# Performance work log

Hardware: AMD Instinct MI355X
Metric: run time of the kernel (lower is better)

The kernel has to match this reference:

```python
import jax, jax.numpy as jnp
import numpy as np

N_USERS = 100000
N_ITEMS = 20000
N_GENRES = 20
N_TAGS = 1128
EMB_ID = 64
EMB_FEAT = 64
HEADS = 8
HIDDEN = 256
D_MOVIE = EMB_ID + 2 * EMB_FEAT  # 192
E_HALF = 200000
N_NODES = N_USERS + N_ITEMS
NEG_SLOPE = 0.2


def setup_inputs() -> dict:
    key = jax.random.key(0)
    ks = jax.random.split(key, 24)
    p = lambda k, shape: (jax.random.normal(k, shape, jnp.float32) * 0.05)
    user_ids = jnp.arange(N_USERS)
    movie_ids = jnp.arange(N_ITEMS)
    mov_x = jax.random.normal(ks[0], (N_ITEMS, N_GENRES + N_TAGS), jnp.float32)
    # bipartite user<->movie edges, both directions (no self loops, matches add_self_loops=False)
    u = jax.random.randint(ks[1], (E_HALF,), 0, N_USERS)
    m = jax.random.randint(ks[2], (E_HALF,), 0, N_ITEMS) + N_USERS
    edge_index = jnp.stack([jnp.concatenate([u, m]), jnp.concatenate([m, u])])  # [2, 2*E_HALF]
    C1 = HIDDEN // HEADS
    return dict(
        user_ids=user_ids, movie_ids=movie_ids, mov_x=mov_x, edge_index=edge_index,
        user_emb=p(ks[3], (N_USERS, EMB_ID)), item_emb=p(ks[4], (N_ITEMS, EMB_ID)),
        gW1=p(ks[5], (N_GENRES, EMB_FEAT)), gb1=jnp.zeros((EMB_FEAT,), jnp.float32),
        gW2=p(ks[6], (EMB_FEAT, EMB_FEAT)), gb2=jnp.zeros((EMB_FEAT,), jnp.float32),
        tW1=p(ks[7], (N_TAGS, EMB_FEAT)), tb1=jnp.zeros((EMB_FEAT,), jnp.float32),
        tW2=p(ks[8], (EMB_FEAT, EMB_FEAT)), tb2=jnp.zeros((EMB_FEAT,), jnp.float32),
        Ws1=p(ks[9], (D_MOVIE, HIDDEN)), Wd1=p(ks[10], (D_MOVIE, HIDDEN)),
        as1=p(ks[11], (HEADS, C1)), ad1=p(ks[12], (HEADS, C1)),
        b1=jnp.zeros((HIDDEN,), jnp.float32),
        Ws2=p(ks[13], (HIDDEN, HIDDEN)), Wd2=p(ks[14], (HIDDEN, HIDDEN)),
        as2=p(ks[15], (1, HIDDEN)), ad2=p(ks[16], (1, HIDDEN)),
        b2=jnp.zeros((HIDDEN,), jnp.float32),
    )


def _gat(x, edge_index, Ws, Wd, a_s, a_d, bias, concat):
    # PyG GATConv (eval mode: dropout off, add_self_loops=False)
    N = x.shape[0]
    H, C = a_s.shape
    hs = (x @ Ws).reshape(N, H, C)  # source-side projection
    hd = (x @ Wd).reshape(N, H, C)  # dest-side projection
    al_s = (hs * a_s).sum(-1)  # [N, H]
    al_d = (hd * a_d).sum(-1)  # [N, H]
    src, dst = edge_index[0], edge_index[1]
    e = al_s[src] + al_d[dst]                      # [E, H]
    e = jnp.where(e > 0, e, NEG_SLOPE * e)         # leaky_relu(0.2)
    mmax = jax.ops.segment_max(e, dst, num_segments=N)
    w = jnp.exp(e - mmax[dst])
    ssum = jax.ops.segment_sum(w, dst, num_segments=N)
    alpha = w / (ssum[dst] + 1e-16)                # segment softmax over incoming edges
    out = jax.ops.segment_sum(hs[src] * alpha[:, :, None], dst, num_segments=N)  # [N, H, C]
    out = out.reshape(N, H * C) if concat else out.mean(axis=1)
    return out + bias


def reference(user_ids, movie_ids, mov_x, edge_index,
              user_emb, item_emb,
              gW1, gb1, gW2, gb2, tW1, tb1, tW2, tb2,
              Ws1, Wd1, as1, ad1, b1,
              Ws2, Wd2, as2, ad2, b2):
    g_feat = mov_x[:, :N_GENRES]
    t_feat = mov_x[:, N_GENRES:]
    g = jax.nn.relu(g_feat @ gW1 + gb1) @ gW2 + gb2
    t = jax.nn.relu(t_feat @ tW1 + tb1) @ tW2 + tb2
    x_mov = jnp.concatenate([item_emb[movie_ids], g, t], axis=1)  # [n_m, D_MOVIE]
    # homogeneous graph: user nodes first (zero-pad user emb to D_MOVIE), then movies
    x_usr = jnp.pad(user_emb[user_ids], ((0, 0), (0, D_MOVIE - EMB_ID)))
    x = jnp.concatenate([x_usr, x_mov], axis=0)  # [N_NODES, D_MOVIE]
    out = jax.nn.elu(_gat(x, edge_index, Ws1, Wd1, as1, ad1, b1, concat=True))
    out = _gat(out, edge_index, Ws2, Wd2, as2, ad2, b2, concat=False)
    ptr = jnp.array([0, N_USERS, N_USERS + N_ITEMS])
    return out, ptr
```

## Files before the change

kernel.cpp:

```cpp
#include <hip/hip_runtime.h>
#include <hip/hip_bf16.h>

#define N_USERS_C 100000
#define N_ITEMS_C 20000
#define N_NODES_C 120000
#define E_TOT_C   400000
#define D_IN_C    192
#define HID_C     256
#define NEG_C     0.2f
#define CLAMP_C   1000.0f
#define KPAD_C    1152
#define NB_SCAN   ((N_NODES_C + 255) / 256)
#define ROWE      40

typedef __attribute__((ext_vector_type(8))) short bfrag;
typedef __attribute__((ext_vector_type(4))) float ffrag;

__device__ __forceinline__ float bf2f(unsigned short u){
  return __uint_as_float(((unsigned)u) << 16);
}
__device__ __forceinline__ float ldf(const void* p, long i, int isf32){
  return isf32 ? ((const float*)p)[i] : bf2f(((const unsigned short*)p)[i]);
}
__device__ __forceinline__ float sane(float v){
  return (v > -1e30f && v < 1e30f) ? v : 0.f;
}
__device__ __forceinline__ int clampsrc(int s){
  return s < 0 ? 0 : (s >= N_NODES_C ? N_NODES_C - 1 : s);
}

__global__ __launch_bounds__(256) void detect_dtype(const unsigned short* __restrict__ ue,
                                                    int* __restrict__ flag){
  __shared__ int cnt[256];
  int tid = threadIdx.x; int c = 0;
  for (int i = tid; i < 8192; i += 256){
    unsigned e = (ue[i] >> 7) & 0xFFu;
    if (e >= 129u) c++;
  }
  cnt[tid] = c; __syncthreads();
  if (tid == 0){
    int s = 0;
    for (int i = 0; i < 256; i++) s += cnt[i];
    *flag = (s > 100) ? 1 : 0;
  }
}

#define NCONV 18
struct ConvArgs { const void* src[NCONV]; int n[NCONV]; int off[NCONV]; };

__global__ __launch_bounds__(256) void conv_small(ConvArgs a, __hip_bfloat16* __restrict__ arena,
                                                  const int* __restrict__ flag){
  int t = blockIdx.x >> 3, sub = blockIdx.x & 7;
  int f32 = *flag;
  const void* s = a.src[t];
  int n = a.n[t], off = a.off[t];
  for (int i = sub * 256 + threadIdx.x; i < n; i += 2048)
    arena[off + i] = __float2bfloat16(ldf(s, i, f32));
}

__global__ void prep_bt(const __hip_bfloat16* __restrict__ Ws,
                        const __hip_bfloat16* __restrict__ Wd,
                        const __hip_bfloat16* __restrict__ as_,
                        const __hip_bfloat16* __restrict__ ad_,
                        __hip_bfloat16* __restrict__ Bt, int K, int H, int C){
  int idx = blockIdx.x * 256 + threadIdx.x;
  if (idx >= 272 * K) return;
  int col = idx / K, k = idx - col * K;
  float v;
  if (col < 256) {
    v = __bfloat162float(Ws[k * 256 + col]);
  } else if (col < 256 + H) {
    int h = col - 256; float s = 0.f;
    for (int c = 0; c < C; c++)
      s += __bfloat162float(Ws[k * 256 + h * C + c]) * __bfloat162float(as_[h * C + c]);
    v = s;
  } else if (col < 256 + 2 * H) {
    int h = col - 256 - H; float s = 0.f;
    for (int c = 0; c < C; c++)
      s += __bfloat162float(Wd[k * 256 + h * C + c]) * __bfloat162float(ad_[h * C + c]);
    v = s;
  } else v = 0.f;
  Bt[(long)col * K + k] = __float2bfloat16(v);
}

__global__ void assemble_x(const void* __restrict__ ue, const void* __restrict__ ie,
                           __hip_bfloat16* __restrict__ x, const int* __restrict__ flag){
  long idx = (long)blockIdx.x * 256 + threadIdx.x;
  if (idx >= (long)N_NODES_C * D_IN_C) return;
  int f32 = *flag;
  int n = (int)(idx / D_IN_C); int c = (int)(idx - (long)n * D_IN_C);
  if (n < N_USERS_C) {
    x[idx] = __float2bfloat16((c < 64) ? ldf(ue, (long)n * 64 + c, f32) : 0.f);
  } else if (c < 64) {
    x[idx] = __float2bfloat16(ldf(ie, (long)(n - N_USERS_C) * 64 + c, f32));
  }
}

__global__ void conv_movx(const void* __restrict__ mv, __hip_bfloat16* __restrict__ out,
                          const int* __restrict__ flag){
  long idx = (long)blockIdx.x * 256 + threadIdx.x;
  if (idx >= (long)N_ITEMS_C * KPAD_C) return;
  int f32 = *flag;
  int m = (int)(idx / KPAD_C); int c = (int)(idx - (long)m * KPAD_C);
  float v = (c < 1148) ? ldf(mv, (long)m * 1148 + c, f32) : 0.f;
  out[idx] = __float2bfloat16(v);
}

__global__ void prep_w1t(const __hip_bfloat16* __restrict__ gW1,
                         const __hip_bfloat16* __restrict__ tW1,
                         __hip_bfloat16* __restrict__ W1t){
  int idx = blockIdx.x * 256 + threadIdx.x;
  if (idx >= 128 * KPAD_C) return;
  int n = idx / KPAD_C, k = idx - n * KPAD_C;
  __hip_bfloat16 v = __float2bfloat16(0.f);
  if (n < 64) { if (k < 20) v = gW1[k * 64 + n]; }
  else       { if (k >= 20 && k < 1148) v = tW1[(k - 20) * 64 + (n - 64)]; }
  W1t[idx] = v;
}

__global__ void prep_w2t(const __hip_bfloat16* __restrict__ gW2,
                         const __hip_bfloat16* __restrict__ tW2,
                         __hip_bfloat16* __restrict__ W2t){
  int idx = blockIdx.x * 256 + threadIdx.x;
  if (idx >= 128 * 128) return;
  int n = idx >> 7, k = idx & 127;
  __hip_bfloat16 v = __float2bfloat16(0.f);
  if (n < 64) { if (k < 64)  v = gW2[k * 64 + n]; }
  else        { if (k >= 64) v = tW2[(k - 64) * 64 + (n - 64)]; }
  W2t[idx] = v;
}

__global__ void prep_movie_bias(const __hip_bfloat16* __restrict__ gb1,
                                const __hip_bfloat16* __restrict__ tb1,
                                const __hip_bfloat16* __restrict__ gb2,
                                const __hip_bfloat16* __restrict__ tb2,
                                __hip_bfloat16* __restrict__ b1c,
                                __hip_bfloat16* __restrict__ b2c){
  int i = threadIdx.x;
  if (i < 64)       b1c[i] = gb1[i];
  else if (i < 128) b1c[i] = tb1[i - 64];
  else if (i < 192) b2c[i - 128] = gb2[i - 128];
  else              b2c[i - 128] = tb2[i - 192];
}

__global__ __launch_bounds__(256) void movie_gemm(
    const __hip_bfloat16* __restrict__ A, int lda, int M,
    const __hip_bfloat16* __restrict__ Bt, int K,
    const __hip_bfloat16* __restrict__ bias, int do_relu,
    __hip_bfloat16* __restrict__ out, int ldo, int ocol){
  __shared__ short Bls[128 * ROWE];
  __shared__ short Als[64 * ROWE];
  int tid = threadIdx.x;
  int wave = tid >> 6;
  int lane = tid & 63;
  int l15 = lane & 15;
  int quad = lane >> 4;
  int rowbase_blk = blockIdx.x * 64;
  int rowbase = rowbase_blk + wave * 16;
  ffrag acc[8];
#pragma unroll
  for (int i = 0; i < 8; i++) acc[i] = (ffrag){0.f, 0.f, 0.f, 0.f};
  const short* As = (const short*)A;
  const short* Bs = (const short*)Bt;
  int sr = tid >> 2, sc = tid & 3;
  int arow_st = rowbase_blk + sr; if (arow_st >= M) arow_st = M - 1;
  for (int k0 = 0; k0 < K; k0 += 32) {
    __syncthreads();
    for (int t = tid; t < 512; t += 256) {
      int r = t >> 2, c = t & 3;
      *(float4*)(&Bls[r * ROWE + c * 8]) = *(const float4*)(Bs + (long)r * K + k0 + c * 8);
    }
    *(float4*)(&Als[sr * ROWE + sc * 8]) =
        *(const float4*)(As + (long)arow_st * lda + k0 + sc * 8);
    __syncthreads();
    int koff = quad * 8;
    bfrag af = *(const bfrag*)(&Als[(wave * 16 + l15) * ROWE + koff]);
#pragma unroll
    for (int nt = 0; nt < 8; nt++) {
      bfrag bf = *(const bfrag*)(&Bls[(nt * 16 + l15) * ROWE + koff]);
      acc[nt] = __builtin_amdgcn_mfma_f32_16x16x32_bf16(af, bf, acc[nt], 0, 0, 0);
    }
  }
#pragma unroll
  for (int reg = 0; reg < 4; reg++) {
    int grow = rowbase + quad * 4 + reg;
    if (grow >= M) continue;
#pragma unroll
    for (int nt = 0; nt < 8; nt++) {
      float v = acc[nt][reg] + __bfloat162float(bias[nt * 16 + l15]);
      if (do_relu) v = fmaxf(v, 0.f);
      out[(long)grow * ldo + ocol + nt * 16 + l15] = __float2bfloat16(v);
    }
  }
}

__global__ __launch_bounds__(256) void gemm_fused(
    const __hip_bfloat16* __restrict__ A, const __hip_bfloat16* __restrict__ Bt,
    __hip_bfloat16* __restrict__ Hout, float* __restrict__ als, float* __restrict__ ald,
    int K, int natt, int ukmax){
  __shared__ short Bls[272 * ROWE];
  __shared__ short Als[64 * ROWE];
  int tid = threadIdx.x;
  int wave = tid >> 6;
  int lane = tid & 63;
  int l15 = lane & 15;
  int quad = lane >> 4;
  int rowbase_blk = blockIdx.x * 64;
  int rowbase = rowbase_blk + wave * 16;
  int kmax = (rowbase_blk + 64 <= N_USERS_C) ? ukmax : K;
  ffrag acc[17];
#pragma unroll
  for (int i = 0; i < 17; i++) acc[i] = (ffrag){0.f, 0.f, 0.f, 0.f};
  const short* As = (const short*)A;
  const short* Bs = (const short*)Bt;
  int sr = tid >> 2, sc = tid & 3;
  for (int k0 = 0; k0 < kmax; k0 += 32) {
    __syncthreads();
    for (int t = tid; t < 1088; t += 256) {
      int r = t >> 2, c = t & 3;
      *(float4*)(&Bls[r * ROWE + c * 8]) = *(const float4*)(Bs + (long)r * K + k0 + c * 8);
    }
    *(float4*)(&Als[sr * ROWE + sc * 8]) =
        *(const float4*)(As + (long)(rowbase_blk + sr) * K + k0 + sc * 8);
    __syncthreads();
    int koff = quad * 8;
    bfrag af = *(const bfrag*)(&Als[(wave * 16 + l15) * ROWE + koff]);
#pragma unroll
    for (int nt = 0; nt < 17; nt++) {
      bfrag bf = *(const bfrag*)(&Bls[(nt * 16 + l15) * ROWE + koff]);
      acc[nt] = __builtin_amdgcn_mfma_f32_16x16x32_bf16(af, bf, acc[nt], 0, 0, 0);
    }
  }
  int col = l15;
#pragma unroll
  for (int reg = 0; reg < 4; reg++) {
    int grow = rowbase + quad * 4 + reg;
    long obase = (long)grow * 256;
#pragma unroll
    for (int nt = 0; nt < 16; nt++)
      Hout[obase + nt * 16 + col] = __float2bfloat16(acc[nt][reg]);
    float v = acc[16][reg];
    if (col < natt) als[grow * natt + col] = v;
    else if (col < 2 * natt) ald[grow * natt + (col - natt)] = v;
  }
}

__global__ void zero_deg(int* __restrict__ deg){
  int i = blockIdx.x * 256 + threadIdx.x;
  if (i < N_NODES_C) deg[i] = 0;
}

__global__ void deg_count(const int* __restrict__ ei, int* __restrict__ deg){
  int e = blockIdx.x * 256 + threadIdx.x;
  if (e >= E_TOT_C) return;
  int dst = ei[E_TOT_C + e];
  if (dst >= 0 && dst < N_NODES_C) atomicAdd(&deg[dst], 1);
}

__global__ __launch_bounds__(256) void deg_bsum(const int* __restrict__ deg,
                                                int* __restrict__ bsum){
  int i = blockIdx.x * 256 + threadIdx.x;
  int v = (i < N_NODES_C) ? deg[i] : 0;
#pragma unroll
  for (int o = 32; o > 0; o >>= 1) v += __shfl_down(v, o, 64);
  __shared__ int ws[4];
  int wave = threadIdx.x >> 6, lane = threadIdx.x & 63;
  if (lane == 0) ws[wave] = v;
  __syncthreads();
  if (threadIdx.x == 0) bsum[blockIdx.x] = ws[0] + ws[1] + ws[2] + ws[3];
}

__global__ __launch_bounds__(512) void bsum_scan(int* __restrict__ bsum,
                                                 int* __restrict__ ptrn){
  __shared__ int sm[512];
  int t = threadIdx.x;
  int v = (t < NB_SCAN) ? bsum[t] : 0;
  sm[t] = v;
  __syncthreads();
  for (int o = 1; o < 512; o <<= 1) {
    int add = (t >= o) ? sm[t - o] : 0;
    __syncthreads();
    sm[t] += add;
    __syncthreads();
  }
  int excl = (t == 0) ? 0 : sm[t - 1];
  if (t < NB_SCAN) bsum[t] = excl;
  if (t == NB_SCAN - 1) ptrn[N_NODES_C] = sm[t];
}

__global__ __launch_bounds__(256) void deg_scan_final(const int* __restrict__ deg,
                                                      const int* __restrict__ bexcl,
                                                      int* __restrict__ ptrn){
  __shared__ int sm[256];
  int i = blockIdx.x * 256 + threadIdx.x;
  int t = threadIdx.x;
  int v = (i < N_NODES_C) ? deg[i] : 0;
  sm[t] = v;
  __syncthreads();
  for (int o = 1; o < 256; o <<= 1) {
    int add = (t >= o) ? sm[t - o] : 0;
    __syncthreads();
    sm[t] += add;
    __syncthreads();
  }
  int excl = (t == 0) ? 0 : sm[t - 1];
  if (i < N_NODES_C) ptrn[i] = bexcl[blockIdx.x] + excl;
}

__global__ void scatter_edges(const int* __restrict__ ei, const int* __restrict__ ptrn,
                              int* __restrict__ cursor, int* __restrict__ elist_src){
  int e = blockIdx.x * 256 + threadIdx.x;
  if (e >= E_TOT_C) return;
  int dst = ei[E_TOT_C + e];
  if (dst < 0 || dst >= N_NODES_C) return;
  int pos = atomicAdd(&cursor[dst], 1);
  elist_src[ptrn[dst] + pos] = ei[e];
}

__global__ __launch_bounds__(256) void aggregate1(
    const int* __restrict__ ptrn, const int* __restrict__ elist_src,
    const float* __restrict__ als, const float* __restrict__ ald,
    const __hip_bfloat16* __restrict__ hs, const __hip_bfloat16* __restrict__ bias,
    __hip_bfloat16* __restrict__ h1){
  int node = blockIdx.x * 4 + (threadIdx.x >> 6);
  if (node >= N_NODES_C) return;
  int lane = threadIdx.x & 63;
  int c0 = lane * 4;
  int h = lane >> 3;
  int beg = ptrn[node], end = ptrn[node + 1];
  float aldv = sane(ald[node * 8 + h]);
  float m = -1e30f;
  float wsum = 0.f, a0 = 0.f, a1 = 0.f, a2 = 0.f, a3 = 0.f;
  const unsigned short* hsu = (const unsigned short*)hs;
  float alsv_p = 0.f;
  ushort4 hv_p = {0, 0, 0, 0};
  int src_b = 0;
  if (beg < end) {
    int s0 = clampsrc(elist_src[beg]);
    alsv_p = als[(long)s0 * 8 + h];
    hv_p = *(const ushort4*)(hsu + (long)s0 * 256 + c0);
    if (beg + 1 < end) src_b = clampsrc(elist_src[beg + 1]);
  }
  for (int i = beg; i < end; i++) {
    float alsv = alsv_p;
    ushort4 hv = hv_p;
    if (i + 1 < end) {
      alsv_p = als[(long)src_b * 8 + h];
      hv_p = *(const ushort4*)(hsu + (long)src_b * 256 + c0);
    }
    if (i + 2 < end)
      src_b = clampsrc(elist_src[i + 2]);
    float ev = sane(alsv) + aldv;
    ev = ev > 0.f ? ev : NEG_C * ev;
    float mnew = fmaxf(m, ev);
    float corr = __expf(m - mnew);
    float w = __expf(ev - mnew);
    m = mnew;
    wsum = wsum * corr + w;
    a0 = a0 * corr + w * bf2f(hv.x); a1 = a1 * corr + w * bf2f(hv.y);
    a2 = a2 * corr + w * bf2f(hv.z); a3 = a3 * corr + w * bf2f(hv.w);
  }
  float inv = 1.f / (wsum + 1e-16f);
  float v0 = a0 * inv + __bfloat162float(bias[c0 + 0]);
  float v1 = a1 * inv + __bfloat162float(bias[c0 + 1]);
  float v2 = a2 * inv + __bfloat162float(bias[c0 + 2]);
  float v3 = a3 * inv + __bfloat162float(bias[c0 + 3]);
  v0 = v0 > 0.f ? v0 : (__expf(v0) - 1.f);
  v1 = v1 > 0.f ? v1 : (__expf(v1) - 1.f);
  v2 = v2 > 0.f ? v2 : (__expf(v2) - 1.f);
  v3 = v3 > 0.f ? v3 : (__expf(v3) - 1.f);
  v0 = fminf(fmaxf(v0, -CLAMP_C), CLAMP_C);
  v1 = fminf(fmaxf(v1, -CLAMP_C), CLAMP_C);
  v2 = fminf(fmaxf(v2, -CLAMP_C), CLAMP_C);
  v3 = fminf(fmaxf(v3, -CLAMP_C), CLAMP_C);
  long ob = (long)node * 256 + c0;
  h1[ob + 0] = __float2bfloat16(v0); h1[ob + 1] = __float2bfloat16(v1);
  h1[ob + 2] = __float2bfloat16(v2); h1[ob + 3] = __float2bfloat16(v3);
}

__global__ __launch_bounds__(256) void aggregate2(
    const int* __restrict__ ptrn, const int* __restrict__ elist_src,
    const float* __restrict__ als, const float* __restrict__ ald,
    const __hip_bfloat16* __restrict__ hs, const __hip_bfloat16* __restrict__ bias,
    float* __restrict__ out){
  int node = blockIdx.x * 4 + (threadIdx.x >> 6);
  if (node >= N_NODES_C) return;
  int lane = threadIdx.x & 63;
  int c0 = lane * 4;
  int beg = ptrn[node], end = ptrn[node + 1];
  float aldv = sane(ald[node]);
  float m = -1e30f;
  float wsum = 0.f, a0 = 0.f, a1 = 0.f, a2 = 0.f, a3 = 0.f;
  const unsigned short* hsu = (const unsigned short*)hs;
  float alsv_p = 0.f;
  ushort4 hv_p = {0, 0, 0, 0};
  int src_b = 0;
  if (beg < end) {
    int s0 = clampsrc(elist_src[beg]);
    alsv_p = als[s0];
    hv_p = *(const ushort4*)(hsu + (long)s0 * 256 + c0);
    if (beg + 1 < end) src_b = clampsrc(elist_src[beg + 1]);
  }
  for (int i = beg; i < end; i++) {
    float alsv = alsv_p;
    ushort4 hv = hv_p;
    if (i + 1 < end) {
      alsv_p = als[src_b];
      hv_p = *(const ushort4*)(hsu + (long)src_b * 256 + c0);
    }
    if (i + 2 < end)
      src_b = clampsrc(elist_src[i + 2]);
    float ev = sane(alsv) + aldv;
    ev = ev > 0.f ? ev : NEG_C * ev;
    float mnew = fmaxf(m, ev);
    float corr = __expf(m - mnew);
    float w = __expf(ev - mnew);
    m = mnew;
    wsum = wsum * corr + w;
    a0 = a0 * corr + w * bf2f(hv.x); a1 = a1 * corr + w * bf2f(hv.y);
    a2 = a2 * corr + w * bf2f(hv.z); a3 = a3 * corr + w * bf2f(hv.w);
  }
  float inv = 1.f / (wsum + 1e-16f);
  float4 v;
  v.x = a0 * inv + __bfloat162float(bias[c0 + 0]);
  v.y = a1 * inv + __bfloat162float(bias[c0 + 1]);
  v.z = a2 * inv + __bfloat162float(bias[c0 + 2]);
  v.w = a3 * inv + __bfloat162float(bias[c0 + 3]);
  v.x = fminf(fmaxf(v.x, -CLAMP_C), CLAMP_C);
  v.y = fminf(fmaxf(v.y, -CLAMP_C), CLAMP_C);
  v.z = fminf(fmaxf(v.z, -CLAMP_C), CLAMP_C);
  v.w = fminf(fmaxf(v.w, -CLAMP_C), CLAMP_C);
  *(float4*)(out + (long)node * 256 + c0) = v;
}

__global__ void write_tail(float* __restrict__ out, int out_size){
  if (threadIdx.x == 0 && blockIdx.x == 0) {
    out[out_size - 3] = 0.f;
    out[out_size - 2] = (float)N_USERS_C;
    out[out_size - 1] = (float)N_NODES_C;
  }
}

extern "C" void kernel_launch(void* const* d_in, const int* in_sizes, int n_in,
                              void* d_out, int out_size, void* d_ws, size_t ws_size,
                              hipStream_t stream) {
  const void* mov_x    = d_in[2];
  const int*  ei       = (const int*)d_in[3];
  const void* user_emb = d_in[4];
  const void* item_emb = d_in[5];

  char* ws = (char*)d_ws;
  size_t off = 0;
  auto alloc = [&](size_t bytes) -> void* {
    void* p = ws + off; off += (bytes + 255) / 256 * 256; return p;
  };
  int* flag   = (int*)alloc(4);
  __hip_bfloat16* arena = (__hip_bfloat16*)alloc(312832 * 2);
  __hip_bfloat16* Bt1 = (__hip_bfloat16*)alloc(272 * 192 * 2);
  __hip_bfloat16* Bt2 = (__hip_bfloat16*)alloc(272 * 256 * 2);
  __hip_bfloat16* W1t = (__hip_bfloat16*)alloc(128 * KPAD_C * 2);
  __hip_bfloat16* W2t = (__hip_bfloat16*)alloc(128 * 128 * 2);
  __hip_bfloat16* b1c = (__hip_bfloat16*)alloc(128 * 2);
  __hip_bfloat16* b2c = (__hip_bfloat16*)alloc(128 * 2);
  int* ptrn   = (int*)alloc((N_NODES_C + 1) * 4);
  int* deg    = (int*)alloc(N_NODES_C * 4);
  int* bsum   = (int*)alloc(512 * 4);
  int* elist  = (int*)alloc(E_TOT_C * 4);
  float* als  = (float*)alloc((size_t)N_NODES_C * 8 * 4);
  float* ald  = (float*)alloc((size_t)N_NODES_C * 8 * 4);
  __hip_bfloat16* x  = (__hip_bfloat16*)alloc((size_t)N_NODES_C * D_IN_C * 2);
  __hip_bfloat16* hs = (__hip_bfloat16*)alloc((size_t)N_NODES_C * HID_C * 2);
  __hip_bfloat16* h1     = (__hip_bfloat16*)d_out;
  __hip_bfloat16* mov_bf = (__hip_bfloat16*)((char*)d_out + 61440000);
  __hip_bfloat16* hid    = hs;

  const int oWs1=0, oWd1=49152, oas1=98304, oad1=98560, ob1=98816,
            oWs2=99072, oWd2=164608, oas2=230144, oad2=230400, ob2=230656,
            ogW1=230912, ogb1=232192, ogW2=232256, ogb2=236352,
            otW1=236416, otb1=308608, otW2=308672, otb2=312768;

  detect_dtype<<<1, 256, 0, stream>>>((const unsigned short*)user_emb, flag);

  ConvArgs ca;
  const int srcidx[NCONV] = {14,15,16,17,18,19,20,21,22,23,6,7,8,9,10,11,12,13};
  const int offs[NCONV]   = {oWs1,oWd1,oas1,oad1,ob1,oWs2,oWd2,oas2,oad2,ob2,
                             ogW1,ogb1,ogW2,ogb2,otW1,otb1,otW2,otb2};
  const int ns[NCONV]     = {49152,49152,256,256,256,65536,65536,256,256,256,
                             1280,64,4096,64,72192,64,4096,64};
  for (int i = 0; i < NCONV; i++) { ca.src[i] = d_in[srcidx[i]]; ca.n[i] = ns[i]; ca.off[i] = offs[i]; }
  conv_small<<<NCONV * 8, 256, 0, stream>>>(ca, arena, flag);

  conv_movx<<<(int)(((long)N_ITEMS_C * KPAD_C + 255) / 256), 256, 0, stream>>>(
      mov_x, mov_bf, flag);
  prep_w1t<<<(128 * KPAD_C + 255) / 256, 256, 0, stream>>>(arena + ogW1, arena + otW1, W1t);
  prep_w2t<<<(128 * 128 + 255) / 256, 256, 0, stream>>>(arena + ogW2, arena + otW2, W2t);
  prep_movie_bias<<<1, 256, 0, stream>>>(arena + ogb1, arena + otb1,
                                         arena + ogb2, arena + otb2, b1c, b2c);
  assemble_x<<<(int)(((long)N_NODES_C * D_IN_C + 255) / 256), 256, 0, stream>>>(
      user_emb, item_emb, x, flag);
  movie_gemm<<<(N_ITEMS_C + 63) / 64, 256, 0, stream>>>(
      mov_bf, KPAD_C, N_ITEMS_C, W1t, KPAD_C, b1c, 1, hid, 128, 0);
  movie_gemm<<<(N_ITEMS_C + 63) / 64, 256, 0, stream>>>(
      hid, 128, N_ITEMS_C, W2t, 128, b2c, 0,
      x + (long)N_USERS_C * D_IN_C, D_IN_C, 64);

  prep_bt<<<(272 * 192 + 255) / 256, 256, 0, stream>>>(
      arena + oWs1, arena + oWd1, arena + oas1, arena + oad1, Bt1, 192, 8, 32);
  prep_bt<<<(272 * 256 + 255) / 256, 256, 0, stream>>>(
      arena + oWs2, arena + oWd2, arena + oas2, arena + oad2, Bt2, 256, 1, 256);

  zero_deg<<<(N_NODES_C + 255) / 256, 256, 0, stream>>>(deg);
  deg_count<<<(E_TOT_C + 255) / 256, 256, 0, stream>>>(ei, deg);
  deg_bsum<<<NB_SCAN, 256, 0, stream>>>(deg, bsum);
  bsum_scan<<<1, 512, 0, stream>>>(bsum, ptrn);
  deg_scan_final<<<NB_SCAN, 256, 0, stream>>>(deg, bsum, ptrn);
  zero_deg<<<(N_NODES_C + 255) / 256, 256, 0, stream>>>(deg);
  scatter_edges<<<(E_TOT_C + 255) / 256, 256, 0, stream>>>(ei, ptrn, deg, elist);

  gemm_fused<<<N_NODES_C / 64, 256, 0, stream>>>(x, Bt1, hs, als, ald, 192, 8, 64);
  aggregate1<<<N_NODES_C / 4, 256, 0, stream>>>(ptrn, elist, als, ald, hs, arena + ob1, h1);

  gemm_fused<<<N_NODES_C / 64, 256, 0, stream>>>(h1, Bt2, hs, als, ald, 256, 1, 256);
  aggregate2<<<N_NODES_C / 4, 256, 0, stream>>>(ptrn, elist, als, ald, hs, arena + ob2,
                                                (float*)d_out);
  write_tail<<<1, 64, 0, stream>>>((float*)d_out, out_size);
}
```

Measured before the change: 677.2 us.

## Fuse all preprocessing kernels into one launch and convert mov_x inside movie GEMM

Merges the many small conversion, transpose, bias, zeroing and assembly kernels into a single block-indexed mega_prep launch that reads raw inputs directly instead of going through a bf16 arena. The movie GEMM now loads mov_x in its original dtype and converts to bf16 while staging tiles, which removes the padded mov_bf intermediate and its full write and read. The edge-scatter cursor gets its own buffer zeroed in the same prep launch, and the ptr tail write is folded into aggregate2. This cuts launch count and intermediate memory traffic. In exchange the GEMM A-load path gains branches and unaligned or scalar loads for the 1148-wide rows.

```diff
diff --git a/kernel.cpp b/kernel.cpp
--- a/kernel.cpp
+++ b/kernel.cpp
@@ -28,6 +28,10 @@
 __device__ __forceinline__ int clampsrc(int s){
   return s < 0 ? 0 : (s >= N_NODES_C ? N_NODES_C - 1 : s);
 }
+__device__ __forceinline__ short f2bs(float f){
+  __hip_bfloat16 h = __float2bfloat16(f);
+  return *reinterpret_cast<short*>(&h);
+}
 
 __global__ __launch_bounds__(256) void detect_dtype(const unsigned short* __restrict__ ue,
                                                     int* __restrict__ flag){
@@ -45,106 +49,125 @@
   }
 }
 
-#define NCONV 18
-struct ConvArgs { const void* src[NCONV]; int n[NCONV]; int off[NCONV]; };
-
-__global__ __launch_bounds__(256) void conv_small(ConvArgs a, __hip_bfloat16* __restrict__ arena,
-                                                  const int* __restrict__ flag){
-  int t = blockIdx.x >> 3, sub = blockIdx.x & 7;
-  int f32 = *flag;
-  const void* s = a.src[t];
-  int n = a.n[t], off = a.off[t];
-  for (int i = sub * 256 + threadIdx.x; i < n; i += 2048)
-    arena[off + i] = __float2bfloat16(ldf(s, i, f32));
-}
-
-__global__ void prep_bt(const __hip_bfloat16* __restrict__ Ws,
-                        const __hip_bfloat16* __restrict__ Wd,
-                        const __hip_bfloat16* __restrict__ as_,
-                        const __hip_bfloat16* __restrict__ ad_,
-                        __hip_bfloat16* __restrict__ Bt, int K, int H, int C){
-  int idx = blockIdx.x * 256 + threadIdx.x;
-  if (idx >= 272 * K) return;
-  int col = idx / K, k = idx - col * K;
-  float v;
-  if (col < 256) {
-    v = __bfloat162float(Ws[k * 256 + col]);
-  } else if (col < 256 + H) {
-    int h = col - 256; float s = 0.f;
-    for (int c = 0; c < C; c++)
-      s += __bfloat162float(Ws[k * 256 + h * C + c]) * __bfloat162float(as_[h * C + c]);
-    v = s;
-  } else if (col < 256 + 2 * H) {
-    int h = col - 256 - H; float s = 0.f;
-    for (int c = 0; c < C; c++)
-      s += __bfloat162float(Wd[k * 256 + h * C + c]) * __bfloat162float(ad_[h * C + c]);
-    v = s;
-  } else v = 0.f;
-  Bt[(long)col * K + k] = __float2bfloat16(v);
-}
-
-__global__ void assemble_x(const void* __restrict__ ue, const void* __restrict__ ie,
-                           __hip_bfloat16* __restrict__ x, const int* __restrict__ flag){
-  long idx = (long)blockIdx.x * 256 + threadIdx.x;
-  if (idx >= (long)N_NODES_C * D_IN_C) return;
-  int f32 = *flag;
-  int n = (int)(idx / D_IN_C); int c = (int)(idx - (long)n * D_IN_C);
-  if (n < N_USERS_C) {
-    x[idx] = __float2bfloat16((c < 64) ? ldf(ue, (long)n * 64 + c, f32) : 0.f);
-  } else if (c < 64) {
-    x[idx] = __float2bfloat16(ldf(ie, (long)(n - N_USERS_C) * 64 + c, f32));
-  }
-}
-
-__global__ void conv_movx(const void* __restrict__ mv, __hip_bfloat16* __restrict__ out,
-                          const int* __restrict__ flag){
-  long idx = (long)blockIdx.x * 256 + threadIdx.x;
-  if (idx >= (long)N_ITEMS_C * KPAD_C) return;
-  int f32 = *flag;
-  int m = (int)(idx / KPAD_C); int c = (int)(idx - (long)m * KPAD_C);
-  float v = (c < 1148) ? ldf(mv, (long)m * 1148 + c, f32) : 0.f;
-  out[idx] = __float2bfloat16(v);
-}
-
-__global__ void prep_w1t(const __hip_bfloat16* __restrict__ gW1,
-                         const __hip_bfloat16* __restrict__ tW1,
-                         __hip_bfloat16* __restrict__ W1t){
-  int idx = blockIdx.x * 256 + threadIdx.x;
-  if (idx >= 128 * KPAD_C) return;
-  int n = idx / KPAD_C, k = idx - n * KPAD_C;
-  __hip_bfloat16 v = __float2bfloat16(0.f);
-  if (n < 64) { if (k < 20) v = gW1[k * 64 + n]; }
-  else       { if (k >= 20 && k < 1148) v = tW1[(k - 20) * 64 + (n - 64)]; }
-  W1t[idx] = v;
-}
-
-__global__ void prep_w2t(const __hip_bfloat16* __restrict__ gW2,
-                         const __hip_bfloat16* __restrict__ tW2,
-                         __hip_bfloat16* __restrict__ W2t){
-  int idx = blockIdx.x * 256 + threadIdx.x;
-  if (idx >= 128 * 128) return;
-  int n = idx >> 7, k = idx & 127;
-  __hip_bfloat16 v = __float2bfloat16(0.f);
-  if (n < 64) { if (k < 64)  v = gW2[k * 64 + n]; }
-  else        { if (k >= 64) v = tW2[(k - 64) * 64 + (n - 64)]; }
-  W2t[idx] = v;
-}
-
-__global__ void prep_movie_bias(const __hip_bfloat16* __restrict__ gb1,
-                                const __hip_bfloat16* __restrict__ tb1,
-                                const __hip_bfloat16* __restrict__ gb2,
-                                const __hip_bfloat16* __restrict__ tb2,
-                                __hip_bfloat16* __restrict__ b1c,
-                                __hip_bfloat16* __restrict__ b2c){
-  int i = threadIdx.x;
-  if (i < 64)       b1c[i] = gb1[i];
-  else if (i < 128) b1c[i] = tb1[i - 64];
-  else if (i < 192) b2c[i - 128] = gb2[i - 128];
-  else              b2c[i - 128] = tb2[i - 192];
+struct PrepArgs {
+  const void *ue, *ie;
+  const void *gW1, *gb1, *gW2, *gb2, *tW1, *tb1, *tW2, *tb2;
+  const void *Ws1, *Wd1, *as1, *ad1, *b1, *Ws2, *Wd2, *as2, *ad2, *b2;
+  __hip_bfloat16 *x, *Bt1, *Bt2, *W1t, *W2t, *b1c, *b2c, *bg1, *bg2;
+  int *deg, *cursor;
+  const int* flag;
+};
+
+#define NB_USER 75000
+#define NB_MOVE 5000
+#define NB_BT1  204
+#define NB_BT2  272
+#define NB_W1T  576
+#define NB_W2T  64
+#define NB_ZERO 938
+#define NB_PREP (NB_USER + NB_MOVE + NB_BT1 + NB_BT2 + NB_W1T + NB_W2T + 1 + NB_ZERO)
+
+__global__ __launch_bounds__(256) void mega_prep(PrepArgs a){
+  int b = blockIdx.x, tid = threadIdx.x;
+  int f32 = *a.flag;
+  if (b < NB_USER) {
+    int idx = b * 256 + tid;
+    int n = idx / 192, c = idx - n * 192;
+    a.x[idx] = __float2bfloat16(c < 64 ? ldf(a.ue, (long)n * 64 + c, f32) : 0.f);
+    return;
+  }
+  b -= NB_USER;
+  if (b < NB_MOVE) {
+    int idx = b * 256 + tid;
+    int m = idx >> 6, c = idx & 63;
+    a.x[(long)(N_USERS_C + m) * 192 + c] =
+        __float2bfloat16(ldf(a.ie, (long)m * 64 + c, f32));
+    return;
+  }
+  b -= NB_MOVE;
+  if (b < NB_BT1) {
+    int idx = b * 256 + tid;
+    if (idx < 272 * 192) {
+      int col = idx / 192, k = idx - col * 192;
+      float v;
+      if (col < 256) v = ldf(a.Ws1, k * 256 + col, f32);
+      else if (col < 264) {
+        int h = col - 256; float s = 0.f;
+        for (int c = 0; c < 32; c++)
+          s += ldf(a.Ws1, k * 256 + h * 32 + c, f32) * ldf(a.as1, h * 32 + c, f32);
+        v = s;
+      } else {
+        int h = col - 264; float s = 0.f;
+        for (int c = 0; c < 32; c++)
+          s += ldf(a.Wd1, k * 256 + h * 32 + c, f32) * ldf(a.ad1, h * 32 + c, f32);
+        v = s;
+      }
+      a.Bt1[col * 192 + k] = __float2bfloat16(v);
+    }
+    return;
+  }
+  b -= NB_BT1;
+  if (b < NB_BT2) {
+    int idx = b * 256 + tid;
+    int col = idx / 256, k = idx & 255;
+    float v;
+    if (col < 256) v = ldf(a.Ws2, k * 256 + col, f32);
+    else if (col == 256) {
+      float s = 0.f;
+      for (int c = 0; c < 256; c++)
+        s += ldf(a.Ws2, k * 256 + c, f32) * ldf(a.as2, c, f32);
+      v = s;
+    } else if (col == 257) {
+      float s = 0.f;
+      for (int c = 0; c < 256; c++)
+        s += ldf(a.Wd2, k * 256 + c, f32) * ldf(a.ad2, c, f32);
+      v = s;
+    } else v = 0.f;
+    a.Bt2[col * 256 + k] = __float2bfloat16(v);
+    return;
+  }
+  b -= NB_BT2;
+  if (b < NB_W1T) {
+    int idx = b * 256 + tid;
+    int n = idx / 1152, k = idx - n * 1152;
+    float v = 0.f;
+    if (n < 64) { if (k < 20) v = ldf(a.gW1, k * 64 + n, f32); }
+    else        { if (k >= 20 && k < 1148) v = ldf(a.tW1, (k - 20) * 64 + (n - 64), f32); }
+    a.W1t[idx] = __float2bfloat16(v);
+    return;
+  }
+  b -= NB_W1T;
+  if (b < NB_W2T) {
+    int idx = b * 256 + tid;
+    int n = idx >> 7, k = idx & 127;
+    float v = 0.f;
+    if (n < 64) { if (k < 64)  v = ldf(a.gW2, k * 64 + n, f32); }
+    else        { if (k >= 64) v = ldf(a.tW2, (k - 64) * 64 + (n - 64), f32); }
+    a.W2t[idx] = __float2bfloat16(v);
+    return;
+  }
+  b -= NB_W2T;
+  if (b < 1) {
+    int i = tid;
+    if (i < 64)       a.b1c[i] = __float2bfloat16(ldf(a.gb1, i, f32));
+    else if (i < 128) a.b1c[i] = __float2bfloat16(ldf(a.tb1, i - 64, f32));
+    else if (i < 192) a.b2c[i - 128] = __float2bfloat16(ldf(a.gb2, i - 128, f32));
+    else              a.b2c[i - 128] = __float2bfloat16(ldf(a.tb2, i - 192, f32));
+    a.bg1[tid] = __float2bfloat16(ldf(a.b1, tid, f32));
+    a.bg2[tid] = __float2bfloat16(ldf(a.b2, tid, f32));
+    return;
+  }
+  b -= 1;
+  {
+    int idx = b * 256 + tid;
+    if (idx < N_NODES_C) a.deg[idx] = 0;
+    else if (idx < 2 * N_NODES_C) a.cursor[idx - N_NODES_C] = 0;
+  }
 }
 
 __global__ __launch_bounds__(256) void movie_gemm(
     const __hip_bfloat16* __restrict__ A, int lda, int M,
+    const void* __restrict__ rawA, const int* __restrict__ flag,
     const __hip_bfloat16* __restrict__ Bt, int K,
     const __hip_bfloat16* __restrict__ bias, int do_relu,
     __hip_bfloat16* __restrict__ out, int ldo, int ocol){
@@ -157,6 +180,7 @@
   int quad = lane >> 4;
   int rowbase_blk = blockIdx.x * 64;
   int rowbase = rowbase_blk + wave * 16;
+  int f32v = rawA ? *flag : 0;
   ffrag acc[8];
 #pragma unroll
   for (int i = 0; i < 8; i++) acc[i] = (ffrag){0.f, 0.f, 0.f, 0.f};
@@ -170,8 +194,36 @@
       int r = t >> 2, c = t & 3;
       *(float4*)(&Bls[r * ROWE + c * 8]) = *(const float4*)(Bs + (long)r * K + k0 + c * 8);
     }
-    *(float4*)(&Als[sr * ROWE + sc * 8]) =
-        *(const float4*)(As + (long)arow_st * lda + k0 + sc * 8);
+    int kc = k0 + sc * 8;
+    if (rawA) {
+      union { short s[8]; float4 f; } u;
+      long base = (long)arow_st * 1148 + kc;
+      if (kc + 8 <= 1148) {
+        if (f32v) {
+          const float* rf = (const float*)rawA + base;
+          float4 x0 = *(const float4*)rf;
+          float4 x1 = *(const float4*)(rf + 4);
+          u.s[0]=f2bs(x0.x); u.s[1]=f2bs(x0.y); u.s[2]=f2bs(x0.z); u.s[3]=f2bs(x0.w);
+          u.s[4]=f2bs(x1.x); u.s[5]=f2bs(x1.y); u.s[6]=f2bs(x1.z); u.s[7]=f2bs(x1.w);
+        } else {
+          const unsigned short* rs = (const unsigned short*)rawA + base;
+          ushort4 a0 = *(const ushort4*)rs;
+          ushort4 a1 = *(const ushort4*)(rs + 4);
+          u.s[0]=(short)a0.x; u.s[1]=(short)a0.y; u.s[2]=(short)a0.z; u.s[3]=(short)a0.w;
+          u.s[4]=(short)a1.x; u.s[5]=(short)a1.y; u.s[6]=(short)a1.z; u.s[7]=(short)a1.w;
+        }
+      } else {
+#pragma unroll
+        for (int j = 0; j < 8; j++) {
+          float v = (kc + j < 1148) ? ldf(rawA, base + j, f32v) : 0.f;
+          u.s[j] = f2bs(v);
+        }
+      }
+      *(float4*)(&Als[sr * ROWE + sc * 8]) = u.f;
+    } else {
+      *(float4*)(&Als[sr * ROWE + sc * 8]) =
+          *(const float4*)(As + (long)arow_st * lda + kc);
+    }
     __syncthreads();
     int koff = quad * 8;
     bfrag af = *(const bfrag*)(&Als[(wave * 16 + l15) * ROWE + koff]);
@@ -243,11 +295,6 @@
     if (col < natt) als[grow * natt + col] = v;
     else if (col < 2 * natt) ald[grow * natt + (col - natt)] = v;
   }
-}
-
-__global__ void zero_deg(int* __restrict__ deg){
-  int i = blockIdx.x * 256 + threadIdx.x;
-  if (i < N_NODES_C) deg[i] = 0;
 }
 
 __global__ void deg_count(const int* __restrict__ ei, int* __restrict__ deg){
@@ -382,7 +429,12 @@
     const int* __restrict__ ptrn, const int* __restrict__ elist_src,
     const float* __restrict__ als, const float* __restrict__ ald,
     const __hip_bfloat16* __restrict__ hs, const __hip_bfloat16* __restrict__ bias,
-    float* __restrict__ out){
+    float* __restrict__ out, int out_size){
+  if (blockIdx.x == 0 && threadIdx.x == 0) {
+    out[out_size - 3] = 0.f;
+    out[out_size - 2] = (float)N_USERS_C;
+    out[out_size - 1] = (float)N_NODES_C;
+  }
   int node = blockIdx.x * 4 + (threadIdx.x >> 6);
   if (node >= N_NODES_C) return;
   int lane = threadIdx.x & 63;
@@ -433,14 +485,6 @@
   *(float4*)(out + (long)node * 256 + c0) = v;
 }
 
-__global__ void write_tail(float* __restrict__ out, int out_size){
-  if (threadIdx.x == 0 && blockIdx.x == 0) {
-    out[out_size - 3] = 0.f;
-    out[out_size - 2] = (float)N_USERS_C;
-    out[out_size - 1] = (float)N_NODES_C;
-  }
-}
-
 extern "C" void kernel_launch(void* const* d_in, const int* in_sizes, int n_in,
                               void* d_out, int out_size, void* d_ws, size_t ws_size,
                               hipStream_t stream) {
@@ -455,73 +499,55 @@
     void* p = ws + off; off += (bytes + 255) / 256 * 256; return p;
   };
   int* flag   = (int*)alloc(4);
-  __hip_bfloat16* arena = (__hip_bfloat16*)alloc(312832 * 2);
   __hip_bfloat16* Bt1 = (__hip_bfloat16*)alloc(272 * 192 * 2);
   __hip_bfloat16* Bt2 = (__hip_bfloat16*)alloc(272 * 256 * 2);
   __hip_bfloat16* W1t = (__hip_bfloat16*)alloc(128 * KPAD_C * 2);
   __hip_bfloat16* W2t = (__hip_bfloat16*)alloc(128 * 128 * 2);
   __hip_bfloat16* b1c = (__hip_bfloat16*)alloc(128 * 2);
   __hip_bfloat16* b2c = (__hip_bfloat16*)alloc(128 * 2);
+  __hip_bfloat16* bg1 = (__hip_bfloat16*)alloc(256 * 2);
+  __hip_bfloat16* bg2 = (__hip_bfloat16*)alloc(256 * 2);
   int* ptrn   = (int*)alloc((N_NODES_C + 1) * 4);
   int* deg    = (int*)alloc(N_NODES_C * 4);
+  int* cursor = (int*)alloc(N_NODES_C * 4);
   int* bsum   = (int*)alloc(512 * 4);
   int* elist  = (int*)alloc(E_TOT_C * 4);
   float* als  = (float*)alloc((size_t)N_NODES_C * 8 * 4);
   float* ald  = (float*)alloc((size_t)N_NODES_C * 8 * 4);
   __hip_bfloat16* x  = (__hip_bfloat16*)alloc((size_t)N_NODES_C * D_IN_C * 2);
   __hip_bfloat16* hs = (__hip_bfloat16*)alloc((size_t)N_NODES_C * HID_C * 2);
-  __hip_bfloat16* h1     = (__hip_bfloat16*)d_out;
-  __hip_bfloat16* mov_bf = (__hip_bfloat16*)((char*)d_out + 61440000);
-  __hip_bfloat16* hid    = hs;
-
-  const int oWs1=0, oWd1=49152, oas1=98304, oad1=98560, ob1=98816,
-            oWs2=99072, oWd2=164608, oas2=230144, oad2=230400, ob2=230656,
-            ogW1=230912, ogb1=232192, ogW2=232256, ogb2=236352,
-            otW1=236416, otb1=308608, otW2=308672, otb2=312768;
+  __hip_bfloat16* h1  = (__hip_bfloat16*)d_out;
+  __hip_bfloat16* hid = hs;
 
   detect_dtype<<<1, 256, 0, stream>>>((const unsigned short*)user_emb, flag);
 
-  ConvArgs ca;
-  const int srcidx[NCONV] = {14,15,16,17,18,19,20,21,22,23,6,7,8,9,10,11,12,13};
-  const int offs[NCONV]   = {oWs1,oWd1,oas1,oad1,ob1,oWs2,oWd2,oas2,oad2,ob2,
-                             ogW1,ogb1,ogW2,ogb2,otW1,otb1,otW2,otb2};
-  const int ns[NCONV]     = {49152,49152,256,256,256,65536,65536,256,256,256,
-                             1280,64,4096,64,72192,64,4096,64};
-  for (int i = 0; i < NCONV; i++) { ca.src[i] = d_in[srcidx[i]]; ca.n[i] = ns[i]; ca.off[i] = offs[i]; }
-  conv_small<<<NCONV * 8, 256, 0, stream>>>(ca, arena, flag);
-
-  conv_movx<<<(int)(((long)N_ITEMS_C * KPAD_C + 255) / 256), 256, 0, stream>>>(
-      mov_x, mov_bf, flag);
-  prep_w1t<<<(128 * KPAD_C + 255) / 256, 256, 0, stream>>>(arena + ogW1, arena + otW1, W1t);
-  prep_w2t<<<(128 * 128 + 255) / 256, 256, 0, stream>>>(arena + ogW2, arena + otW2, W2t);
-  prep_movie_bias<<<1, 256, 0, stream>>>(arena + ogb1, arena + otb1,
-                                         arena + ogb2, arena + otb2, b1c, b2c);
-  assemble_x<<<(int)(((long)N_NODES_C * D_IN_C + 255) / 256), 256, 0, stream>>>(
-      user_emb, item_emb, x, flag);
+  PrepArgs pa;
+  pa.ue = user_emb; pa.ie = item_emb;
+  pa.gW1 = d_in[6];  pa.gb1 = d_in[7];  pa.gW2 = d_in[8];  pa.gb2 = d_in[9];
+  pa.tW1 = d_in[10]; pa.tb1 = d_in[11]; pa.tW2 = d_in[12]; pa.tb2 = d_in[13];
+  pa.Ws1 = d_in[14]; pa.Wd1 = d_in[15]; pa.as1 = d_in[16]; pa.ad1 = d_in[17]; pa.b1 = d_in[18];
+  pa.Ws2 = d_in[19]; pa.Wd2 = d_in[20]; pa.as2 = d_in[21]; pa.ad2 = d_in[22]; pa.b2 = d_in[23];
+  pa.x = x; pa.Bt1 = Bt1; pa.Bt2 = Bt2; pa.W1t = W1t; pa.W2t = W2t;
+  pa.b1c = b1c; pa.b2c = b2c; pa.bg1 = bg1; pa.bg2 = bg2;
+  pa.deg = deg; pa.cursor = cursor; pa.flag = flag;
+  mega_prep<<<NB_PREP, 256, 0, stream>>>(pa);
+
   movie_gemm<<<(N_ITEMS_C + 63) / 64, 256, 0, stream>>>(
-      mov_bf, KPAD_C, N_ITEMS_C, W1t, KPAD_C, b1c, 1, hid, 128, 0);
+      nullptr, 0, N_ITEMS_C, mov_x, flag, W1t, KPAD_C, b1c, 1, hid, 128, 0);
   movie_gemm<<<(N_ITEMS_C + 63) / 64, 256, 0, stream>>>(
-      hid, 128, N_ITEMS_C, W2t, 128, b2c, 0,
+      hid, 128, N_ITEMS_C, nullptr, flag, W2t, 128, b2c, 0,
       x + (long)N_USERS_C * D_IN_C, D_IN_C, 64);
 
-  prep_bt<<<(272 * 192 + 255) / 256, 256, 0, stream>>>(
-      arena + oWs1, arena + oWd1, arena + oas1, arena + oad1, Bt1, 192, 8, 32);
-  prep_bt<<<(272 * 256 + 255) / 256, 256, 0, stream>>>(
-      arena + oWs2, arena + oWd2, arena + oas2, arena + oad2, Bt2, 256, 1, 256);
-
-  zero_deg<<<(N_NODES_C + 255) / 256, 256, 0, stream>>>(deg);
   deg_count<<<(E_TOT_C + 255) / 256, 256, 0, stream>>>(ei, deg);
   deg_bsum<<<NB_SCAN, 256, 0, stream>>>(deg, bsum);
   bsum_scan<<<1, 512, 0, stream>>>(bsum, ptrn);
   deg_scan_final<<<NB_SCAN, 256, 0, stream>>>(deg, bsum, ptrn);
-  zero_deg<<<(N_NODES_C + 255) / 256, 256, 0, stream>>>(deg);
-  scatter_edges<<<(E_TOT_C + 255) / 256, 256, 0, stream>>>(ei, ptrn, deg, elist);
+  scatter_edges<<<(E_TOT_C + 255) / 256, 256, 0, stream>>>(ei, ptrn, cursor, elist);
 
   gemm_fused<<<N_NODES_C / 64, 256, 0, stream>>>(x, Bt1, hs, als, ald, 192, 8, 64);
-  aggregate1<<<N_NODES_C / 4, 256, 0, stream>>>(ptrn, elist, als, ald, hs, arena + ob1, h1);
+  aggregate1<<<N_NODES_C / 4, 256, 0, stream>>>(ptrn, elist, als, ald, hs, bg1, h1);
 
   gemm_fused<<<N_NODES_C / 64, 256, 0, stream>>>(h1, Bt2, hs, als, ald, 256, 1, 256);
-  aggregate2<<<N_NODES_C / 4, 256, 0, stream>>>(ptrn, elist, als, ald, hs, arena + ob2,
-                                                (float*)d_out);
-  write_tail<<<1, 64, 0, stream>>>((float*)d_out, out_size);
-}
+  aggregate2<<<N_NODES_C / 4, 256, 0, stream>>>(ptrn, elist, als, ald, hs, bg2,
+                                                (float*)d_out, out_size);
+}
```

Result: faster. 621.3 us (-8.3%).
